# Kernel optimization log

Hardware: AMD Instinct MI355X
Metric: run time of the kernel (lower is better)

The kernel has to match this reference:

```python
import jax, jax.numpy as jnp
import numpy as np

B, S, F, H, O, L, HORIZON = 64, 512, 512, 1024, 512, 2, 1


def setup_inputs() -> dict:
    key = jax.random.key(0)
    ks = jax.random.split(key, 11)
    s0 = 1.0 / np.sqrt(F + H)   # torch Linear default init scale (uniform-ish)
    s1 = 1.0 / np.sqrt(H + H)
    sf = 1.0 / np.sqrt(H)
    return {
        "x":   jax.random.normal(ks[0], (B, S, F), jnp.float32),
        "Wf0": jax.random.normal(ks[1], (F + H, H), jnp.float32) * s0,
        "bf0": jax.random.normal(ks[2], (H,), jnp.float32) * s0,
        "Wc0": jax.random.normal(ks[3], (F + H, H), jnp.float32) * s0,
        "bc0": jax.random.normal(ks[4], (H,), jnp.float32) * s0,
        "Wf1": jax.random.normal(ks[5], (H + H, H), jnp.float32) * s1,
        "bf1": jax.random.normal(ks[6], (H,), jnp.float32) * s1,
        "Wc1": jax.random.normal(ks[7], (H + H, H), jnp.float32) * s1,
        "bc1": jax.random.normal(ks[8], (H,), jnp.float32) * s1,
        "Wfc": jax.random.normal(ks[9], (H, O), jnp.float32) * sf,
        "bfc": jax.random.normal(ks[10], (O,), jnp.float32) * sf,
    }


def _janet_forward(x, Wf, bf, Wc, bc, Wfc, bfc):
    # x: [B, S, F] -> scan over time with stacked JANET cells.
    xt = jnp.swapaxes(x, 0, 1)  # [S, B, F]
    h0 = tuple(jnp.zeros((x.shape[0], H), x.dtype) for _ in range(L))
    c0 = tuple(jnp.zeros((x.shape[0], H), x.dtype) for _ in range(L))

    def step(carry, x_t):
        hs, cs = carry
        inp = x_t
        new_h, new_c = [], []
        for l in range(L):
            comb = jnp.concatenate([inp, hs[l]], axis=1)      # [B, in+H]
            f_t = jax.nn.sigmoid(comb @ Wf[l] + bf[l])        # forget gate
            c_tilde = jnp.tanh(comb @ Wc[l] + bc[l])
            c_t = f_t * cs[l] + (1.0 - f_t) * c_tilde
            h_t = jnp.tanh(c_t)
            new_h.append(h_t)
            new_c.append(c_t)
            inp = h_t
        return (tuple(new_h), tuple(new_c)), new_h[-1]

    _, h_seq = jax.lax.scan(step, (h0, c0), xt)               # [S, B, H]
    h_seq = jnp.swapaxes(h_seq, 0, 1)                          # [B, S, H]
    tail = h_seq[:, -HORIZON:, :]                              # dropout is eval-mode identity
    return tail @ Wfc + bfc                                    # [B, HORIZON, O]


def reference(x, Wf0, bf0, Wc0, bc0, Wf1, bf1, Wc1, bc1, Wfc, bfc):
    return _janet_forward(x, (Wf0, Wf1), (bf0, bf1), (Wc0, Wc1), (bc0, bc1), Wfc, bfc)
```

## Files before the change

kernel.cpp:

```cpp
#include <hip/hip_runtime.h>
#include <stdint.h>

typedef _Float16 f16;
typedef _Float16 f16x8 __attribute__((ext_vector_type(8)));
typedef float    f32x4 __attribute__((ext_vector_type(4)));

#define Bm 64
#define Ss 512
#define Ff 512
#define Hh 1024
#define Oo 512
#define NWG 256
#define HBh (Bm*Hh)
#define SLOTB (HBh*2)

#define FL0_U32 0
#define FL1_U32 4096
#define NSLOT 8
#define H0F_BYTE ((size_t)65536)
#define H1F_BYTE (H0F_BYTE + (size_t)NSLOT*SLOTB)

#define MFMA16 __builtin_amdgcn_mfma_f32_16x16x32_f16

__device__ __forceinline__ float sigm(float x){ return 1.0f/(1.0f+__expf(-x)); }
__device__ __forceinline__ float tanhf_(float x){
  x = fminf(15.0f, fmaxf(-15.0f, x));
  float e = __expf(-2.0f*x);
  return (1.0f - e)/(1.0f + e);
}

__global__ void init_fresh(void* ws){
  const uint4 z = {0,0,0,0};
  int idx = blockIdx.x*blockDim.x + threadIdx.x;
  const int total = 4096 + 8192 + 8192;
  for (int i = idx; i < total; i += gridDim.x*blockDim.x) {
    if (i < 4096)        ((uint4*)ws)[i] = z;
    else if (i < 12288)  ((uint4*)((char*)ws + H0F_BYTE + (size_t)7*SLOTB))[i-4096]  = z;
    else                 ((uint4*)((char*)ws + H1F_BYTE + (size_t)7*SLOTB))[i-12288] = z;
  }
}

__device__ __forceinline__ void setflag(unsigned* p, unsigned v){
  asm volatile("global_atomic_swap %0, %1, off" :: "v"(p), "v"(v) : "memory");
}

__device__ __forceinline__ void poll2(unsigned* wsu, int fb0, unsigned tgt0,
                                      int fb1, unsigned tgt1, int tid){
  if (tid < 64) {
    const unsigned* p0 = wsu + fb0 + 16*tid;
    const unsigned* p1 = wsu + fb1 + 16*tid;
    for (;;) {
      unsigned v0, v1;
      asm volatile("global_load_dword %0, %2, off sc0 sc1\n\t"
                   "global_load_dword %1, %3, off sc0 sc1\n\t"
                   "s_waitcnt vmcnt(0)"
                   : "=&v"(v0), "=&v"(v1) : "v"(p0), "v"(p1) : "memory");
      if (__all((v0 >= tgt0) && (v1 >= tgt1))) break;
      __builtin_amdgcn_s_sleep(1);
    }
  }
  asm volatile("s_waitcnt vmcnt(0)" ::: "memory");
  __builtin_amdgcn_sched_barrier(0);
  __syncthreads();
}

#define ISSUE8T(A, P0, P1, P2, P3) asm volatile( \
  "global_load_dwordx4 %0, %8, off offset:-4096 sc0 sc1\n\t" \
  "global_load_dwordx4 %1, %8, off sc0 sc1\n\t" \
  "global_load_dwordx4 %2, %9, off offset:-4096 sc0 sc1\n\t" \
  "global_load_dwordx4 %3, %9, off sc0 sc1\n\t" \
  "global_load_dwordx4 %4, %10, off offset:-4096 sc0 sc1\n\t" \
  "global_load_dwordx4 %5, %10, off sc0 sc1\n\t" \
  "global_load_dwordx4 %6, %11, off offset:-4096 sc0 sc1\n\t" \
  "global_load_dwordx4 %7, %11, off sc0 sc1" \
  : "=&v"(A[0]), "=&v"(A[1]), "=&v"(A[2]), "=&v"(A[3]), \
    "=&v"(A[4]), "=&v"(A[5]), "=&v"(A[6]), "=&v"(A[7]) \
  : "v"(P0), "v"(P1), "v"(P2), "v"(P3) : "memory")

#define WAITV(N) do{ asm volatile("s_waitcnt vmcnt(" #N ")" ::: "memory"); \
                     __builtin_amdgcn_sched_barrier(0x106); }while(0)

#define CONS8D(Aarr, KSB, KSC) do{ \
  _Pragma("unroll") \
  for (int j = 0; j < 8; ++j){ \
    f16x8 bw = ldsA[(size_t)((KSB)+j)*64]; \
    f16x8 cw = ldsA[(size_t)((KSC)+(KSB)+j)*64]; \
    if (j & 1){ aF1 = MFMA16(Aarr[j], bw, aF1, 0,0,0); aC1 = MFMA16(Aarr[j], cw, aC1, 0,0,0); } \
    else      { aF0 = MFMA16(Aarr[j], bw, aF0, 0,0,0); aC0 = MFMA16(Aarr[j], cw, aC0, 0,0,0); } \
  } \
}while(0)

__device__ __forceinline__ f16x8 cvt8(float4 v0, float4 v1){
  f16x8 a;
  a[0]=v0.x; a[1]=v0.y; a[2]=v0.z; a[3]=v0.w;
  a[4]=v1.x; a[5]=v1.y; a[6]=v1.z; a[7]=v1.w;
  return a;
}

__global__ __launch_bounds__(256,1) void janet_persistent(
    const float* __restrict__ x,
    const float* __restrict__ Wf0, const float* __restrict__ bf0,
    const float* __restrict__ Wc0, const float* __restrict__ bc0,
    const float* __restrict__ Wf1, const float* __restrict__ bf1,
    const float* __restrict__ Wc1, const float* __restrict__ bc1,
    const float* __restrict__ Wfc, const float* __restrict__ bfc,
    float* __restrict__ out, void* __restrict__ ws)
{
  __shared__ __align__(16) unsigned char smem[135168];
  __builtin_amdgcn_fence(__ATOMIC_ACQUIRE, "agent");

  unsigned* wsu = (unsigned*)ws;
  char* h0base = (char*)ws + H0F_BYTE;
  char* h1base = (char*)ws + H1F_BYTE;

  const int wid  = blockIdx.x;
  const int tid  = threadIdx.x;
  const bool isL0 = (wid < 128);
  const int half = (wid >> 6) & 1;
  const int lw   = wid & 63;
  const int col0 = lw * 16;
  const int K    = isL0 ? (Ff + Hh) : (2*Hh);
  const int KS   = K >> 5;

  {
    const float* Wg[2] = { isL0 ? Wf0 : Wf1, isL0 ? Wc0 : Wc1 };
    for (int g = 0; g < 2; ++g) {
      const float* W = Wg[g];
      for (int e = tid; e < 16*K; e += 256) {
        int n = e & 15, k = e >> 4;
        float v = W[(size_t)k*Hh + col0 + n];
        int ks = k >> 5, sub = (k >> 3) & 3, j = k & 7;
        int lane = n + (sub << 4);
        int byte = ((g*KS + ks) << 10) + (lane << 4) + (j << 1);
        *(f16*)(smem + byte) = (f16)v;
      }
    }
  }
  __syncthreads();

  const int lane = tid & 63;
  const int wv   = tid >> 6;
  const int rt   = wv & 1;
  const int kh   = wv >> 1;
  const int n    = lane & 15;
  const int kg   = lane >> 4;
  const int e8   = kg * 8;
  const int lrow = rt*16 + n;
  const int grow = half*32 + lrow;
  const int part = n & 3;
  const int rsel = n >> 2;
  const int srowl = rt*16 + 4*kg + rsel;

  const float* bfp = isL0 ? bf0 : bf1;
  const float* bcp = isL0 ? bc0 : bc1;
  const float bfv = bfp[col0 + n];
  const float bcv = bcp[col0 + n];

  const f16x8* ldsA = (const f16x8*)(smem + (size_t)lane*16);
  const size_t rdoff = (size_t)(kg>>1)*2048 + (size_t)half*1024
                     + (size_t)lrow*32 + (size_t)(kg&1)*16 + 4096;
  float* xchg = (float*)(smem + 131072 + rt*2048 + lane*32);

  const int fl0 = FL0_U32 + (half*64)*16;
  const int fl1 = FL1_U32 + (half*64)*16;

  f32x4 cst = {0.f,0.f,0.f,0.f};

  if (isL0) {
    for (int t = 0; t < Ss; ++t) {
      f32x4 aF0={0.f,0.f,0.f,0.f}, aF1={0.f,0.f,0.f,0.f};
      f32x4 aC0={0.f,0.f,0.f,0.f}, aC1={0.f,0.f,0.f,0.f};
      const float* xb = x + ((size_t)grow*Ss + (size_t)t)*Ff + (size_t)kh*256 + e8;
      float4 xv0[8], xv1[8];
      #pragma unroll
      for (int i = 0; i < 8; ++i) {
        xv0[i] = *(const float4*)(xb + 32*i);
        xv1[i] = *(const float4*)(xb + 32*i + 4);
      }
      #pragma unroll
      for (int i = 0; i < 8; ++i) {
        f16x8 a  = cvt8(xv0[i], xv1[i]);
        int ks = kh*8 + i;
        f16x8 bw = ldsA[(size_t)ks*64];
        f16x8 cw = ldsA[(size_t)(48 + ks)*64];
        if (i & 1){ aF1 = MFMA16(a, bw, aF1, 0,0,0); aC1 = MFMA16(a, cw, aC1, 0,0,0); }
        else      { aF0 = MFMA16(a, bw, aF0, 0,0,0); aC0 = MFMA16(a, cw, aC0, 0,0,0); }
      }
      poll2(wsu, fl0, (unsigned)t, fl1, t >= 8 ? (unsigned)(t-7) : 0u, tid);
      const char* hb = h0base + (size_t)((t+7)&7)*SLOTB + rdoff + (size_t)kh*65536;
      f16x8 A0[8], A1[8];
      __builtin_amdgcn_sched_barrier(0);
      ISSUE8T(A0, hb,       hb+8192,  hb+16384, hb+24576);
      ISSUE8T(A1, hb+32768, hb+40960, hb+49152, hb+57344);
      WAITV(8); CONS8D(A0, 16 + kh*16, 48);
      WAITV(0); CONS8D(A1, 24 + kh*16, 48);
      f32x4 pF = aF0 + aF1, pC = aC0 + aC1;
      if (kh == 1) { *(f32x4*)xchg = pF; *(f32x4*)(xchg+4) = pC; }
      __syncthreads();
      if (kh == 0) {
        pF += *(const f32x4*)xchg;
        pC += *(const f32x4*)(xchg+4);
        unsigned cu[4];
        #pragma unroll
        for (int j = 0; j < 4; ++j) {
          float f  = sigm(pF[j] + bfv);
          float ct = tanhf_(pC[j] + bcv);
          cst[j] = f*cst[j] + (1.0f - f)*ct;
          union { _Float16 h; unsigned short u; } cv; cv.h = (f16)tanhf_(cst[j]);
          cu[j] = cv.u;
        }
        unsigned u01 = cu[0] | (cu[1] << 16);
        unsigned u23 = cu[2] | (cu[3] << 16);
        int sb = (kg << 4) + (part << 2);
        unsigned wsel[4];
        #pragma unroll
        for (int i = 0; i < 4; ++i) {
          unsigned w01 = __shfl(u01, sb + i, 64);
          unsigned w23 = __shfl(u23, sb + i, 64);
          unsigned w = (rsel < 2) ? w01 : w23;
          wsel[i] = (rsel & 1) ? (w >> 16) : (w & 0xffffu);
        }
        unsigned d0 = wsel[0] | (wsel[1] << 16);
        unsigned d1 = wsel[2] | (wsel[3] << 16);
        uint64_t dd = (uint64_t)d0 | ((uint64_t)d1 << 32);
        char* hd = h0base + (size_t)(t&7)*SLOTB + (size_t)lw*2048
                 + (size_t)half*1024 + (size_t)srowl*32 + (size_t)part*8;
        asm volatile("global_atomic_swap_x2 %0, %1, off" :: "v"(hd), "v"(dd) : "memory");
      }
      asm volatile("s_waitcnt vmcnt(0)" ::: "memory");
      __syncthreads();
      if (tid == 0) setflag(wsu + FL0_U32 + (half*64 + lw)*16, (unsigned)(t+1));
    }
  } else {
    for (int s = 0; s < Ss; ++s) {
      poll2(wsu, fl0, (unsigned)(s+1), fl1, (unsigned)s, tid);
      f32x4 aF0={0.f,0.f,0.f,0.f}, aF1={0.f,0.f,0.f,0.f};
      f32x4 aC0={0.f,0.f,0.f,0.f}, aC1={0.f,0.f,0.f,0.f};
      const char* hb = (kh == 0)
        ? h0base + (size_t)(s&7)*SLOTB + rdoff
        : h1base + (size_t)((s+7)&7)*SLOTB + rdoff;
      f16x8 A0[8], A1[8], A2[8], A3[8];
      __builtin_amdgcn_sched_barrier(0);
      ISSUE8T(A0, hb,       hb+8192,  hb+16384, hb+24576);
      ISSUE8T(A1, hb+32768, hb+40960, hb+49152, hb+57344);
      ISSUE8T(A2, hb+65536, hb+73728, hb+81920, hb+90112);
      ISSUE8T(A3, hb+98304, hb+106496, hb+114688, hb+122880);
      {
        const int kb = kh*32;
        WAITV(24); CONS8D(A0, kb + 0,  64);
        WAITV(16); CONS8D(A1, kb + 8,  64);
        WAITV(8);  CONS8D(A2, kb + 16, 64);
        WAITV(0);  CONS8D(A3, kb + 24, 64);
      }
      f32x4 pF = aF0 + aF1, pC = aC0 + aC1;
      if (kh == 1) { *(f32x4*)xchg = pF; *(f32x4*)(xchg+4) = pC; }
      __syncthreads();
      if (kh == 0) {
        pF += *(const f32x4*)xchg;
        pC += *(const f32x4*)(xchg+4);
        unsigned cu[4];
        #pragma unroll
        for (int j = 0; j < 4; ++j) {
          float f  = sigm(pF[j] + bfv);
          float ct = tanhf_(pC[j] + bcv);
          cst[j] = f*cst[j] + (1.0f - f)*ct;
          union { _Float16 h; unsigned short u; } cv; cv.h = (f16)tanhf_(cst[j]);
          cu[j] = cv.u;
        }
        unsigned u01 = cu[0] | (cu[1] << 16);
        unsigned u23 = cu[2] | (cu[3] << 16);
        int sb = (kg << 4) + (part << 2);
        unsigned wsel[4];
        #pragma unroll
        for (int i = 0; i < 4; ++i) {
          unsigned w01 = __shfl(u01, sb + i, 64);
          unsigned w23 = __shfl(u23, sb + i, 64);
          unsigned w = (rsel < 2) ? w01 : w23;
          wsel[i] = (rsel & 1) ? (w >> 16) : (w & 0xffffu);
        }
        unsigned d0 = wsel[0] | (wsel[1] << 16);
        unsigned d1 = wsel[2] | (wsel[3] << 16);
        uint64_t dd = (uint64_t)d0 | ((uint64_t)d1 << 32);
        char* hd = h1base + (size_t)(s&7)*SLOTB + (size_t)lw*2048
                 + (size_t)half*1024 + (size_t)srowl*32 + (size_t)part*8;
        asm volatile("global_atomic_swap_x2 %0, %1, off" :: "v"(hd), "v"(dd) : "memory");
      }
      asm volatile("s_waitcnt vmcnt(0)" ::: "memory");
      __syncthreads();
      if (tid == 0) setflag(wsu + FL1_U32 + (half*64 + lw)*16, (unsigned)(s+1));
    }
  }

  poll2(wsu, FL1_U32, (unsigned)Ss, FL1_U32 + 64*16, (unsigned)Ss, tid);
  if (tid < 128) {
    const char* fin = h1base + (size_t)7*SLOTB;
    const int o = wid*2 + (tid & 1);
    const int b = tid >> 1;
    const char* rowp = fin + (size_t)(b>>5)*1024 + (size_t)(b&31)*32;
    float acc = bfc[o];
    for (int cg = 0; cg < 64; ++cg) {
      f16x8 lo, hi;
      asm volatile("global_load_dwordx4 %0, %2, off sc0 sc1\n\t"
                   "global_load_dwordx4 %1, %2, off offset:16 sc0 sc1\n\t"
                   "s_waitcnt vmcnt(0)"
                   : "=&v"(lo), "=&v"(hi) : "v"(rowp + (size_t)cg*2048) : "memory");
      #pragma unroll
      for (int i = 0; i < 8; ++i) {
        acc += (float)lo[i] * Wfc[(size_t)(cg*16 + i)*Oo + o];
        acc += (float)hi[i] * Wfc[(size_t)(cg*16 + 8 + i)*Oo + o];
      }
    }
    out[(size_t)b*Oo + o] = acc;
  }
}

extern "C" void kernel_launch(void* const* d_in, const int* in_sizes, int n_in,
                              void* d_out, int out_size, void* d_ws, size_t ws_size,
                              hipStream_t stream) {
  const float* x   = (const float*)d_in[0];
  const float* Wf0 = (const float*)d_in[1];
  const float* bf0 = (const float*)d_in[2];
  const float* Wc0 = (const float*)d_in[3];
  const float* bc0 = (const float*)d_in[4];
  const float* Wf1 = (const float*)d_in[5];
  const float* bf1 = (const float*)d_in[6];
  const float* Wc1 = (const float*)d_in[7];
  const float* bc1 = (const float*)d_in[8];
  const float* Wfc = (const float*)d_in[9];
  const float* bfc = (const float*)d_in[10];

  init_fresh<<<64, 256, 0, stream>>>(d_ws);
  janet_persistent<<<NWG, 256, 0, stream>>>(x, Wf0, bf0, Wc0, bc0,
                                            Wf1, bf1, Wc1, bc1, Wfc, bfc,
                                            (float*)d_out, d_ws);
}
```

Baseline: 2.538 ms.

## Use per-timestep hidden-state slots to drop reuse polling and cache bypass

Replaces the 8-slot ring buffer for hidden states with one slot per timestep (513 slots), so layer 0 no longer has to poll layer 1's progress before overwriting a slot and only waits on its own flags. Because no slot is ever rewritten, the h loads drop the sc0 sc1 cache-coherence bits and go through normal caching. The LDS exchange for the F and C partial sums is also split into two separate arrays. The trade-off is a much larger workspace (about 128 MB). Dropping the coherence bits risks reading stale lines if any cache level still holds data from before the producer's write.

```diff
diff --git a/kernel.cpp b/kernel.cpp
--- a/kernel.cpp
+++ b/kernel.cpp
@@ -16,9 +16,10 @@
 
 #define FL0_U32 0
 #define FL1_U32 4096
-#define NSLOT 8
+#define NSLOT 513
 #define H0F_BYTE ((size_t)65536)
 #define H1F_BYTE (H0F_BYTE + (size_t)NSLOT*SLOTB)
+#define WSF_NEED (H1F_BYTE + (size_t)NSLOT*SLOTB)
 
 #define MFMA16 __builtin_amdgcn_mfma_f32_16x16x32_f16
 
@@ -35,13 +36,30 @@
   const int total = 4096 + 8192 + 8192;
   for (int i = idx; i < total; i += gridDim.x*blockDim.x) {
     if (i < 4096)        ((uint4*)ws)[i] = z;
-    else if (i < 12288)  ((uint4*)((char*)ws + H0F_BYTE + (size_t)7*SLOTB))[i-4096]  = z;
-    else                 ((uint4*)((char*)ws + H1F_BYTE + (size_t)7*SLOTB))[i-12288] = z;
+    else if (i < 12288)  ((uint4*)((char*)ws + H0F_BYTE))[i-4096]  = z;
+    else                 ((uint4*)((char*)ws + H1F_BYTE))[i-12288] = z;
   }
 }
 
 __device__ __forceinline__ void setflag(unsigned* p, unsigned v){
   asm volatile("global_atomic_swap %0, %1, off" :: "v"(p), "v"(v) : "memory");
+}
+
+__device__ __forceinline__ void poll1(unsigned* wsu, int fb, unsigned tgt, int tid){
+  if (tid < 64) {
+    const unsigned* p0 = wsu + fb + 16*tid;
+    for (;;) {
+      unsigned v0;
+      asm volatile("global_load_dword %0, %1, off sc0 sc1\n\t"
+                   "s_waitcnt vmcnt(0)"
+                   : "=&v"(v0) : "v"(p0) : "memory");
+      if (__all(v0 >= tgt)) break;
+      __builtin_amdgcn_s_sleep(1);
+    }
+  }
+  asm volatile("s_waitcnt vmcnt(0)" ::: "memory");
+  __builtin_amdgcn_sched_barrier(0);
+  __syncthreads();
 }
 
 __device__ __forceinline__ void poll2(unsigned* wsu, int fb0, unsigned tgt0,
@@ -65,14 +83,14 @@
 }
 
 #define ISSUE8T(A, P0, P1, P2, P3) asm volatile( \
-  "global_load_dwordx4 %0, %8, off offset:-4096 sc0 sc1\n\t" \
-  "global_load_dwordx4 %1, %8, off sc0 sc1\n\t" \
-  "global_load_dwordx4 %2, %9, off offset:-4096 sc0 sc1\n\t" \
-  "global_load_dwordx4 %3, %9, off sc0 sc1\n\t" \
-  "global_load_dwordx4 %4, %10, off offset:-4096 sc0 sc1\n\t" \
-  "global_load_dwordx4 %5, %10, off sc0 sc1\n\t" \
-  "global_load_dwordx4 %6, %11, off offset:-4096 sc0 sc1\n\t" \
-  "global_load_dwordx4 %7, %11, off sc0 sc1" \
+  "global_load_dwordx4 %0, %8, off offset:-4096\n\t" \
+  "global_load_dwordx4 %1, %8, off\n\t" \
+  "global_load_dwordx4 %2, %9, off offset:-4096\n\t" \
+  "global_load_dwordx4 %3, %9, off\n\t" \
+  "global_load_dwordx4 %4, %10, off offset:-4096\n\t" \
+  "global_load_dwordx4 %5, %10, off\n\t" \
+  "global_load_dwordx4 %6, %11, off offset:-4096\n\t" \
+  "global_load_dwordx4 %7, %11, off" \
   : "=&v"(A[0]), "=&v"(A[1]), "=&v"(A[2]), "=&v"(A[3]), \
     "=&v"(A[4]), "=&v"(A[5]), "=&v"(A[6]), "=&v"(A[7]) \
   : "v"(P0), "v"(P1), "v"(P2), "v"(P3) : "memory")
@@ -159,7 +177,8 @@
   const f16x8* ldsA = (const f16x8*)(smem + (size_t)lane*16);
   const size_t rdoff = (size_t)(kg>>1)*2048 + (size_t)half*1024
                      + (size_t)lrow*32 + (size_t)(kg&1)*16 + 4096;
-  float* xchg = (float*)(smem + 131072 + rt*2048 + lane*32);
+  float* xchgF = (float*)(smem + 131072 + rt*1024 + lane*16);
+  float* xchgC = (float*)(smem + 133120 + rt*1024 + lane*16);
 
   const int fl0 = FL0_U32 + (half*64)*16;
   const int fl1 = FL1_U32 + (half*64)*16;
@@ -186,8 +205,8 @@
         if (i & 1){ aF1 = MFMA16(a, bw, aF1, 0,0,0); aC1 = MFMA16(a, cw, aC1, 0,0,0); }
         else      { aF0 = MFMA16(a, bw, aF0, 0,0,0); aC0 = MFMA16(a, cw, aC0, 0,0,0); }
       }
-      poll2(wsu, fl0, (unsigned)t, fl1, t >= 8 ? (unsigned)(t-7) : 0u, tid);
-      const char* hb = h0base + (size_t)((t+7)&7)*SLOTB + rdoff + (size_t)kh*65536;
+      poll1(wsu, fl0, (unsigned)t, tid);
+      const char* hb = h0base + (size_t)t*SLOTB + rdoff + (size_t)kh*65536;
       f16x8 A0[8], A1[8];
       __builtin_amdgcn_sched_barrier(0);
       ISSUE8T(A0, hb,       hb+8192,  hb+16384, hb+24576);
@@ -195,11 +214,11 @@
       WAITV(8); CONS8D(A0, 16 + kh*16, 48);
       WAITV(0); CONS8D(A1, 24 + kh*16, 48);
       f32x4 pF = aF0 + aF1, pC = aC0 + aC1;
-      if (kh == 1) { *(f32x4*)xchg = pF; *(f32x4*)(xchg+4) = pC; }
+      if (kh == 1) { *(f32x4*)xchgF = pF; *(f32x4*)xchgC = pC; }
       __syncthreads();
       if (kh == 0) {
-        pF += *(const f32x4*)xchg;
-        pC += *(const f32x4*)(xchg+4);
+        pF += *(const f32x4*)xchgF;
+        pC += *(const f32x4*)xchgC;
         unsigned cu[4];
         #pragma unroll
         for (int j = 0; j < 4; ++j) {
@@ -223,7 +242,7 @@
         unsigned d0 = wsel[0] | (wsel[1] << 16);
         unsigned d1 = wsel[2] | (wsel[3] << 16);
         uint64_t dd = (uint64_t)d0 | ((uint64_t)d1 << 32);
-        char* hd = h0base + (size_t)(t&7)*SLOTB + (size_t)lw*2048
+        char* hd = h0base + (size_t)(t+1)*SLOTB + (size_t)lw*2048
                  + (size_t)half*1024 + (size_t)srowl*32 + (size_t)part*8;
         asm volatile("global_atomic_swap_x2 %0, %1, off" :: "v"(hd), "v"(dd) : "memory");
       }
@@ -237,8 +256,8 @@
       f32x4 aF0={0.f,0.f,0.f,0.f}, aF1={0.f,0.f,0.f,0.f};
       f32x4 aC0={0.f,0.f,0.f,0.f}, aC1={0.f,0.f,0.f,0.f};
       const char* hb = (kh == 0)
-        ? h0base + (size_t)(s&7)*SLOTB + rdoff
-        : h1base + (size_t)((s+7)&7)*SLOTB + rdoff;
+        ? h0base + (size_t)(s+1)*SLOTB + rdoff
+        : h1base + (size_t)s*SLOTB + rdoff;
       f16x8 A0[8], A1[8], A2[8], A3[8];
       __builtin_amdgcn_sched_barrier(0);
       ISSUE8T(A0, hb,       hb+8192,  hb+16384, hb+24576);
@@ -253,11 +272,11 @@
         WAITV(0);  CONS8D(A3, kb + 24, 64);
       }
       f32x4 pF = aF0 + aF1, pC = aC0 + aC1;
-      if (kh == 1) { *(f32x4*)xchg = pF; *(f32x4*)(xchg+4) = pC; }
+      if (kh == 1) { *(f32x4*)xchgF = pF; *(f32x4*)xchgC = pC; }
       __syncthreads();
       if (kh == 0) {
-        pF += *(const f32x4*)xchg;
-        pC += *(const f32x4*)(xchg+4);
+        pF += *(const f32x4*)xchgF;
+        pC += *(const f32x4*)xchgC;
         unsigned cu[4];
         #pragma unroll
         for (int j = 0; j < 4; ++j) {
@@ -281,7 +300,7 @@
         unsigned d0 = wsel[0] | (wsel[1] << 16);
         unsigned d1 = wsel[2] | (wsel[3] << 16);
         uint64_t dd = (uint64_t)d0 | ((uint64_t)d1 << 32);
-        char* hd = h1base + (size_t)(s&7)*SLOTB + (size_t)lw*2048
+        char* hd = h1base + (size_t)(s+1)*SLOTB + (size_t)lw*2048
                  + (size_t)half*1024 + (size_t)srowl*32 + (size_t)part*8;
         asm volatile("global_atomic_swap_x2 %0, %1, off" :: "v"(hd), "v"(dd) : "memory");
       }
@@ -293,7 +312,7 @@
 
   poll2(wsu, FL1_U32, (unsigned)Ss, FL1_U32 + 64*16, (unsigned)Ss, tid);
   if (tid < 128) {
-    const char* fin = h1base + (size_t)7*SLOTB;
+    const char* fin = h1base + (size_t)Ss*SLOTB;
     const int o = wid*2 + (tid & 1);
     const int b = tid >> 1;
     const char* rowp = fin + (size_t)(b>>5)*1024 + (size_t)(b&31)*32;
```

New measurement: 2.449 ms. 3.5% less time.
